# Performance work log

Measured on AMD Instinct MI355X. Metric: run time of the kernel, lower is better.

The kernel has to match this reference:

```python
import jax, jax.numpy as jnp
import numpy as np

TRACT_SPECS = [
    dict(name="x_a", src_size=4096, dst_size=1024, connections=64, seed=42),
    dict(name="x_b", src_size=4096, dst_size=512, connections=64, seed=43),
    dict(name="x_c", src_size=2048, dst_size=512, connections=32, seed=44),
]


def _make_mask(dst_size, src_size, n_conn, seed):
    rng = np.random.RandomState(seed)
    mask = np.zeros((dst_size, src_size), dtype=np.float32)
    for dst in range(dst_size):
        idx = rng.choice(src_size, size=min(n_conn, src_size), replace=False)
        mask[dst, idx] = 1.0
    return jnp.asarray(mask)


def _xavier_uniform(key, dst, src):
    # matches nn.init.xavier_uniform_ for a (dst, src) weight
    limit = float(np.sqrt(6.0 / (dst + src)))
    return jax.random.uniform(key, (dst, src), jnp.float32, -limit, limit)


def setup_inputs() -> dict:
    key = jax.random.key(0)
    keys = jax.random.split(key, 6)
    B, S = 8, 1024
    inp = {}
    for i, spec in enumerate(TRACT_SPECS):
        src, dst = spec["src_size"], spec["dst_size"]
        inp[spec["name"]] = jax.random.normal(keys[i], (B, S, src), jnp.float32)
        inp["w_" + spec["name"][-1]] = _xavier_uniform(keys[3 + i], dst, src)
        inp["m_" + spec["name"][-1]] = _make_mask(dst, src, spec["connections"], spec["seed"])
    return inp


def reference(x_a, x_b, x_c, w_a, w_b, w_c, m_a, m_b, m_c):
    # Each tract: F.linear(x, weight * mask) -> x @ (W*M)^T; then concat on last dim.
    out_a = jnp.einsum("bsi,oi->bso", x_a, w_a * m_a)
    out_b = jnp.einsum("bsi,oi->bso", x_b, w_b * m_b)
    out_c = jnp.einsum("bsi,oi->bso", x_c, w_c * m_c)
    return jnp.concatenate([out_a, out_b, out_c], axis=-1)
```

## Files before the change

kernel.cpp:

```cpp
#include <hip/hip_runtime.h>
#include <hip/hip_fp16.h>
#include <stdint.h>


#define BS_TOTAL 8192
#define SRC_A 4096
#define SRC_B 4096
#define SRC_C 2048
#define DST_A 1024
#define DST_B 512
#define DST_C 512
#define K_A 64
#define K_B 64
#define K_C 32
#define OUT_DIM 2048

#define PAIR_XB_OFF 4096
#define PAIR_XC_OFF 8192
#define PAIR_TOT 10240
#define LDS_BYTES (PAIR_TOT * 8)

typedef float f32x4 __attribute__((ext_vector_type(4)));


__global__ __launch_bounds__(256) void compress_kernel(
    const float* __restrict__ w_a, const float* __restrict__ m_a,
    const float* __restrict__ w_b, const float* __restrict__ m_b,
    const float* __restrict__ w_c, const float* __restrict__ m_c,
    unsigned* __restrict__ pa, unsigned* __restrict__ pb,
    unsigned* __restrict__ pc) {
    __shared__ int s_cnt;
    __shared__ int s_idx[64];
    __shared__ float s_w[64];
    __shared__ int s_bankcnt[16];
    __shared__ int s_bankoff[16];
    __shared__ unsigned s_sorted[64];

    const int blk = blockIdx.x;
    const int t = threadIdx.x;

    const float *w, *m;
    unsigned* p;
    int dst, src_n, K, DST, pair_off;
    if (blk < DST_A) {
        w = w_a; m = m_a; p = pa; dst = blk;
        src_n = SRC_A; K = K_A; DST = DST_A; pair_off = 0;
    } else if (blk < DST_A + DST_B) {
        w = w_b; m = m_b; p = pb; dst = blk - DST_A;
        src_n = SRC_B; K = K_B; DST = DST_B; pair_off = PAIR_XB_OFF;
    } else {
        w = w_c; m = m_c; p = pc; dst = blk - DST_A - DST_B;
        src_n = SRC_C; K = K_C; DST = DST_C; pair_off = PAIR_XC_OFF;
    }

    if (t == 0) s_cnt = 0;
    if (t < 16) s_bankcnt[t] = 0;
    __syncthreads();

    const float* mrow = m + (size_t)dst * src_n;
    const float* wrow = w + (size_t)dst * src_n;
    const int per_thread = src_n >> 8;
    for (int i = 0; i < per_thread; ++i) {
        int e = t + (i << 8);
        float mv = mrow[e];
        if (mv != 0.0f) {
            int pos = atomicAdd(&s_cnt, 1);
            if (pos < 64) {
                s_idx[pos] = e;
                s_w[pos] = wrow[e] * mv;
            }
        }
    }
    __syncthreads();
    int cnt = s_cnt;
    if (cnt > K) cnt = K;

    if (t < cnt) atomicAdd(&s_bankcnt[s_idx[t] & 15], 1);
    __syncthreads();
    if (t == 0) {
        int acc = 0;
        for (int b = 0; b < 16; ++b) {
            s_bankoff[b] = acc;
            acc += s_bankcnt[b];
        }
    }
    __syncthreads();
    if (t < cnt) {
        int idx = s_idx[t];
        int j = atomicAdd(&s_bankoff[idx & 15], 1);
        unsigned hb = (unsigned)__half_as_ushort(__float2half(s_w[t]));
        s_sorted[j] = ((unsigned)(pair_off + idx) << 16) | hb;
    }
    __syncthreads();
    if (t >= cnt && t < K) s_sorted[t] = ((unsigned)pair_off << 16);
    __syncthreads();

    if (t < K) {
        int rot = (K == 64) ? ((dst & 15) << 2) : ((dst & 15) << 1);
        unsigned v = s_sorted[(t + rot) % K];
        p[(((t >> 2) * DST) + dst) * 4 + (t & 3)] = v;
    }
}

__global__ __launch_bounds__(256, 2) void tract_kernel(
    const float* __restrict__ x_a, const float* __restrict__ x_b,
    const float* __restrict__ x_c,
    const unsigned* __restrict__ pa, const unsigned* __restrict__ pb,
    const unsigned* __restrict__ pc,
    float* __restrict__ out) {
    extern __shared__ unsigned xs[];
    const int t = threadIdx.x;
    const size_t r0 = (size_t)blockIdx.x * 4;

    const f32x4* a0 = (const f32x4*)(x_a + (r0 + 0) * SRC_A);
    const f32x4* a1 = (const f32x4*)(x_a + (r0 + 1) * SRC_A);
    const f32x4* a2 = (const f32x4*)(x_a + (r0 + 2) * SRC_A);
    const f32x4* a3 = (const f32x4*)(x_a + (r0 + 3) * SRC_A);
    const f32x4* b0 = (const f32x4*)(x_b + (r0 + 0) * SRC_B);
    const f32x4* b1 = (const f32x4*)(x_b + (r0 + 1) * SRC_B);
    const f32x4* b2 = (const f32x4*)(x_b + (r0 + 2) * SRC_B);
    const f32x4* b3 = (const f32x4*)(x_b + (r0 + 3) * SRC_B);
    const f32x4* c0 = (const f32x4*)(x_c + (r0 + 0) * SRC_C);
    const f32x4* c1 = (const f32x4*)(x_c + (r0 + 1) * SRC_C);
    const f32x4* c2 = (const f32x4*)(x_c + (r0 + 2) * SRC_C);
    const f32x4* c3 = (const f32x4*)(x_c + (r0 + 3) * SRC_C);
    uint4* xs4 = (uint4*)xs;

#pragma unroll
    for (int i = 0; i < 10; ++i) {
        int q = t + (i << 8);
        const f32x4 *s0, *s1, *s2, *s3;
        int qo;
        if (q < 1024)      { s0 = a0; s1 = a1; s2 = a2; s3 = a3; qo = q; }
        else if (q < 2048) { s0 = b0; s1 = b1; s2 = b2; s3 = b3; qo = q - 1024; }
        else               { s0 = c0; s1 = c1; s2 = c2; s3 = c3; qo = q - 2048; }
        f32x4 v0 = s0[qo];
        f32x4 v1 = s1[qo];
        f32x4 v2 = s2[qo];
        f32x4 v3 = s3[qo];
        uint4 w0, w1;
        __half2 h;
        h = __floats2half2_rn(v0.x, v1.x); w0.x = *(unsigned*)&h;
        h = __floats2half2_rn(v2.x, v3.x); w0.y = *(unsigned*)&h;
        h = __floats2half2_rn(v0.y, v1.y); w0.z = *(unsigned*)&h;
        h = __floats2half2_rn(v2.y, v3.y); w0.w = *(unsigned*)&h;
        h = __floats2half2_rn(v0.z, v1.z); w1.x = *(unsigned*)&h;
        h = __floats2half2_rn(v2.z, v3.z); w1.y = *(unsigned*)&h;
        h = __floats2half2_rn(v0.w, v1.w); w1.z = *(unsigned*)&h;
        h = __floats2half2_rn(v2.w, v3.w); w1.w = *(unsigned*)&h;
        xs4[2 * q]     = w0;
        xs4[2 * q + 1] = w1;
    }
    __syncthreads();

    const uint2* xp = (const uint2*)xs;
    float* o0 = out + (r0 + 0) * OUT_DIM;
    float* o1 = out + (r0 + 1) * OUT_DIM;
    float* o2 = out + (r0 + 2) * OUT_DIM;
    float* o3 = out + (r0 + 3) * OUT_DIM;

#define PROC(u) {                                                            \
        uint2 xv = xp[(u) >> 16];                                            \
        float w = __half2float(__ushort_as_half((unsigned short)((u) & 0xffffu))); \
        const __half2 hlo = *(const __half2*)&xv.x;                          \
        const __half2 hhi = *(const __half2*)&xv.y;                          \
        acc0 = fmaf(w, __low2float(hlo), acc0);                              \
        acc1 = fmaf(w, __high2float(hlo), acc1);                             \
        acc2 = fmaf(w, __low2float(hhi), acc2);                              \
        acc3 = fmaf(w, __high2float(hhi), acc3); }

    const uint4* ta = (const uint4*)pa;
    const uint4* tb = (const uint4*)pb;
    const uint4* tc = (const uint4*)pc;

#pragma unroll 1
    for (int o = 0; o < 4; ++o) {
        int dst = t + (o << 8);
        float acc0 = 0.0f, acc1 = 0.0f, acc2 = 0.0f, acc3 = 0.0f;
#pragma unroll
        for (int k4 = 0; k4 < (K_A >> 2); ++k4) {
            uint4 e = ta[k4 * DST_A + dst];
            PROC(e.x) PROC(e.y) PROC(e.z) PROC(e.w)
        }
        __builtin_nontemporal_store(acc0, o0 + dst);
        __builtin_nontemporal_store(acc1, o1 + dst);
        __builtin_nontemporal_store(acc2, o2 + dst);
        __builtin_nontemporal_store(acc3, o3 + dst);
    }
#pragma unroll 1
    for (int o = 0; o < 2; ++o) {
        int dst = t + (o << 8);
        float acc0 = 0.0f, acc1 = 0.0f, acc2 = 0.0f, acc3 = 0.0f;
#pragma unroll
        for (int k4 = 0; k4 < (K_B >> 2); ++k4) {
            uint4 e = tb[k4 * DST_B + dst];
            PROC(e.x) PROC(e.y) PROC(e.z) PROC(e.w)
        }
        __builtin_nontemporal_store(acc0, o0 + DST_A + dst);
        __builtin_nontemporal_store(acc1, o1 + DST_A + dst);
        __builtin_nontemporal_store(acc2, o2 + DST_A + dst);
        __builtin_nontemporal_store(acc3, o3 + DST_A + dst);
    }
#pragma unroll 1
    for (int o = 0; o < 2; ++o) {
        int dst = t + (o << 8);
        float acc0 = 0.0f, acc1 = 0.0f, acc2 = 0.0f, acc3 = 0.0f;
#pragma unroll
        for (int k4 = 0; k4 < (K_C >> 2); ++k4) {
            uint4 e = tc[k4 * DST_C + dst];
            PROC(e.x) PROC(e.y) PROC(e.z) PROC(e.w)
        }
        __builtin_nontemporal_store(acc0, o0 + DST_A + DST_B + dst);
        __builtin_nontemporal_store(acc1, o1 + DST_A + DST_B + dst);
        __builtin_nontemporal_store(acc2, o2 + DST_A + DST_B + dst);
        __builtin_nontemporal_store(acc3, o3 + DST_A + DST_B + dst);
    }
#undef PROC
}

extern "C" void kernel_launch(void* const* d_in, const int* in_sizes, int n_in,
                              void* d_out, int out_size, void* d_ws, size_t ws_size,
                              hipStream_t stream) {
    const float* x_a = (const float*)d_in[0];
    const float* w_a = (const float*)d_in[1];
    const float* m_a = (const float*)d_in[2];
    const float* x_b = (const float*)d_in[3];
    const float* w_b = (const float*)d_in[4];
    const float* m_b = (const float*)d_in[5];
    const float* x_c = (const float*)d_in[6];
    const float* w_c = (const float*)d_in[7];
    const float* m_c = (const float*)d_in[8];
    float* out = (float*)d_out;

    char* ws = (char*)d_ws;
    unsigned* pa = (unsigned*)(ws);
    unsigned* pb = (unsigned*)(ws + 262144);
    unsigned* pc = (unsigned*)(ws + 262144 + 131072);

    static bool configured = false;
    if (!configured) {
        hipFuncSetAttribute(reinterpret_cast<const void*>(&tract_kernel),
                            hipFuncAttributeMaxDynamicSharedMemorySize, LDS_BYTES);
        configured = true;
    }

    compress_kernel<<<DST_A + DST_B + DST_C, 256, 0, stream>>>(
        w_a, m_a, w_b, m_b, w_c, m_c, pa, pb, pc);
    tract_kernel<<<BS_TOTAL / 4, 256, LDS_BYTES, stream>>>(x_a, x_b, x_c, pa, pb, pc, out);
}
```

Before: 411.5 us.

## Split tract kernel into per-tract blocks with smaller LDS footprint

The fused kernel is restructured so each block handles a single tract for 4 rows instead of all three tracts. The LDS tile shrinks from 80KB to 32KB and the grid triples, allowing more resident blocks per CU and better latency hiding. The compress kernel now loads the mask with vector loads and fetches weights only for nonzero entries. In exchange, each block does less work, so launch and sync overhead rise, and the per-block blocks are uneven across tracts.

```diff
diff --git a/kernel.cpp b/kernel.cpp
--- a/kernel.cpp
+++ b/kernel.cpp
@@ -14,11 +14,12 @@
 #define K_B 64
 #define K_C 32
 #define OUT_DIM 2048
-
-#define PAIR_XB_OFF 4096
-#define PAIR_XC_OFF 8192
-#define PAIR_TOT 10240
-#define LDS_BYTES (PAIR_TOT * 8)
+#define ROWS 4
+
+#define NBLK_A (BS_TOTAL / ROWS)
+#define NBLK_B (BS_TOTAL / ROWS)
+#define NBLK_C (BS_TOTAL / ROWS)
+#define LDS_BYTES (SRC_A * 8)
 
 typedef float f32x4 __attribute__((ext_vector_type(4)));
 
@@ -31,7 +32,6 @@
     unsigned* __restrict__ pc) {
     __shared__ int s_cnt;
     __shared__ int s_idx[64];
-    __shared__ float s_w[64];
     __shared__ int s_bankcnt[16];
     __shared__ int s_bankoff[16];
     __shared__ unsigned s_sorted[64];
@@ -41,16 +41,16 @@
 
     const float *w, *m;
     unsigned* p;
-    int dst, src_n, K, DST, pair_off;
+    int dst, src_n, K, DST;
     if (blk < DST_A) {
         w = w_a; m = m_a; p = pa; dst = blk;
-        src_n = SRC_A; K = K_A; DST = DST_A; pair_off = 0;
+        src_n = SRC_A; K = K_A; DST = DST_A;
     } else if (blk < DST_A + DST_B) {
         w = w_b; m = m_b; p = pb; dst = blk - DST_A;
-        src_n = SRC_B; K = K_B; DST = DST_B; pair_off = PAIR_XB_OFF;
+        src_n = SRC_B; K = K_B; DST = DST_B;
     } else {
         w = w_c; m = m_c; p = pc; dst = blk - DST_A - DST_B;
-        src_n = SRC_C; K = K_C; DST = DST_C; pair_off = PAIR_XC_OFF;
+        src_n = SRC_C; K = K_C; DST = DST_C;
     }
 
     if (t == 0) s_cnt = 0;
@@ -59,15 +59,16 @@
 
     const float* mrow = m + (size_t)dst * src_n;
     const float* wrow = w + (size_t)dst * src_n;
-    const int per_thread = src_n >> 8;
-    for (int i = 0; i < per_thread; ++i) {
-        int e = t + (i << 8);
-        float mv = mrow[e];
-        if (mv != 0.0f) {
-            int pos = atomicAdd(&s_cnt, 1);
-            if (pos < 64) {
-                s_idx[pos] = e;
-                s_w[pos] = wrow[e] * mv;
+    const f32x4* m4 = (const f32x4*)mrow;
+    const int nq = src_n >> 10;
+    for (int i = 0; i < nq; ++i) {
+        int q = t + (i << 8);
+        f32x4 mv = m4[q];
+#pragma unroll
+        for (int j = 0; j < 4; ++j) {
+            if (mv[j] != 0.0f) {
+                int pos = atomicAdd(&s_cnt, 1);
+                if (pos < 64) s_idx[pos] = 4 * q + j;
             }
         }
     }
@@ -88,56 +89,50 @@
     if (t < cnt) {
         int idx = s_idx[t];
         int j = atomicAdd(&s_bankoff[idx & 15], 1);
-        unsigned hb = (unsigned)__half_as_ushort(__float2half(s_w[t]));
-        s_sorted[j] = ((unsigned)(pair_off + idx) << 16) | hb;
-    }
-    __syncthreads();
-    if (t >= cnt && t < K) s_sorted[t] = ((unsigned)pair_off << 16);
+        float wv = wrow[idx] * mrow[idx];
+        unsigned hb = (unsigned)__half_as_ushort(__float2half(wv));
+        s_sorted[j] = ((unsigned)idx << 16) | hb;
+    }
+    __syncthreads();
+    if (t >= cnt && t < K) s_sorted[t] = 0u;
     __syncthreads();
 
     if (t < K) {
         int rot = (K == 64) ? ((dst & 15) << 2) : ((dst & 15) << 1);
-        unsigned v = s_sorted[(t + rot) % K];
+        unsigned v = s_sorted[(t + rot) & (K - 1)];
         p[(((t >> 2) * DST) + dst) * 4 + (t & 3)] = v;
     }
 }
 
-__global__ __launch_bounds__(256, 2) void tract_kernel(
-    const float* __restrict__ x_a, const float* __restrict__ x_b,
-    const float* __restrict__ x_c,
-    const unsigned* __restrict__ pa, const unsigned* __restrict__ pb,
-    const unsigned* __restrict__ pc,
-    float* __restrict__ out) {
-    extern __shared__ unsigned xs[];
-    const int t = threadIdx.x;
-    const size_t r0 = (size_t)blockIdx.x * 4;
-
-    const f32x4* a0 = (const f32x4*)(x_a + (r0 + 0) * SRC_A);
-    const f32x4* a1 = (const f32x4*)(x_a + (r0 + 1) * SRC_A);
-    const f32x4* a2 = (const f32x4*)(x_a + (r0 + 2) * SRC_A);
-    const f32x4* a3 = (const f32x4*)(x_a + (r0 + 3) * SRC_A);
-    const f32x4* b0 = (const f32x4*)(x_b + (r0 + 0) * SRC_B);
-    const f32x4* b1 = (const f32x4*)(x_b + (r0 + 1) * SRC_B);
-    const f32x4* b2 = (const f32x4*)(x_b + (r0 + 2) * SRC_B);
-    const f32x4* b3 = (const f32x4*)(x_b + (r0 + 3) * SRC_B);
-    const f32x4* c0 = (const f32x4*)(x_c + (r0 + 0) * SRC_C);
-    const f32x4* c1 = (const f32x4*)(x_c + (r0 + 1) * SRC_C);
-    const f32x4* c2 = (const f32x4*)(x_c + (r0 + 2) * SRC_C);
-    const f32x4* c3 = (const f32x4*)(x_c + (r0 + 3) * SRC_C);
+
+#define PROC(u) {                                                            \
+        uint2 xv = xp[(u) >> 16];                                            \
+        float w = __half2float(__ushort_as_half((unsigned short)((u) & 0xffffu))); \
+        const __half2 hlo = *(const __half2*)&xv.x;                          \
+        const __half2 hhi = *(const __half2*)&xv.y;                          \
+        acc0 = fmaf(w, __low2float(hlo), acc0);                              \
+        acc1 = fmaf(w, __high2float(hlo), acc1);                             \
+        acc2 = fmaf(w, __low2float(hhi), acc2);                              \
+        acc3 = fmaf(w, __high2float(hhi), acc3); }
+
+template <int SRCN, int KQ, int DSTN, int NOUT>
+__device__ __forceinline__ void do_tract(
+    const float* __restrict__ xsrc, const uint4* __restrict__ tab,
+    float* __restrict__ outb,
+    size_t r0, int t, unsigned* xs) {
+    const f32x4* s0 = (const f32x4*)(xsrc + (r0 + 0) * SRCN);
+    const f32x4* s1 = (const f32x4*)(xsrc + (r0 + 1) * SRCN);
+    const f32x4* s2 = (const f32x4*)(xsrc + (r0 + 2) * SRCN);
+    const f32x4* s3 = (const f32x4*)(xsrc + (r0 + 3) * SRCN);
     uint4* xs4 = (uint4*)xs;
 
 #pragma unroll
-    for (int i = 0; i < 10; ++i) {
+    for (int i = 0; i < (SRCN >> 10); ++i) {
         int q = t + (i << 8);
-        const f32x4 *s0, *s1, *s2, *s3;
-        int qo;
-        if (q < 1024)      { s0 = a0; s1 = a1; s2 = a2; s3 = a3; qo = q; }
-        else if (q < 2048) { s0 = b0; s1 = b1; s2 = b2; s3 = b3; qo = q - 1024; }
-        else               { s0 = c0; s1 = c1; s2 = c2; s3 = c3; qo = q - 2048; }
-        f32x4 v0 = s0[qo];
-        f32x4 v1 = s1[qo];
-        f32x4 v2 = s2[qo];
-        f32x4 v3 = s3[qo];
+        f32x4 v0 = s0[q];
+        f32x4 v1 = s1[q];
+        f32x4 v2 = s2[q];
+        f32x4 v3 = s3[q];
         uint4 w0, w1;
         __half2 h;
         h = __floats2half2_rn(v0.x, v1.x); w0.x = *(unsigned*)&h;
@@ -154,32 +149,18 @@
     __syncthreads();
 
     const uint2* xp = (const uint2*)xs;
-    float* o0 = out + (r0 + 0) * OUT_DIM;
-    float* o1 = out + (r0 + 1) * OUT_DIM;
-    float* o2 = out + (r0 + 2) * OUT_DIM;
-    float* o3 = out + (r0 + 3) * OUT_DIM;
-
-#define PROC(u) {                                                            \
-        uint2 xv = xp[(u) >> 16];                                            \
-        float w = __half2float(__ushort_as_half((unsigned short)((u) & 0xffffu))); \
-        const __half2 hlo = *(const __half2*)&xv.x;                          \
-        const __half2 hhi = *(const __half2*)&xv.y;                          \
-        acc0 = fmaf(w, __low2float(hlo), acc0);                              \
-        acc1 = fmaf(w, __high2float(hlo), acc1);                             \
-        acc2 = fmaf(w, __low2float(hhi), acc2);                              \
-        acc3 = fmaf(w, __high2float(hhi), acc3); }
-
-    const uint4* ta = (const uint4*)pa;
-    const uint4* tb = (const uint4*)pb;
-    const uint4* tc = (const uint4*)pc;
+    float* o0 = outb;
+    float* o1 = outb + OUT_DIM;
+    float* o2 = outb + 2 * OUT_DIM;
+    float* o3 = outb + 3 * OUT_DIM;
 
 #pragma unroll 1
-    for (int o = 0; o < 4; ++o) {
+    for (int o = 0; o < NOUT; ++o) {
         int dst = t + (o << 8);
         float acc0 = 0.0f, acc1 = 0.0f, acc2 = 0.0f, acc3 = 0.0f;
 #pragma unroll
-        for (int k4 = 0; k4 < (K_A >> 2); ++k4) {
-            uint4 e = ta[k4 * DST_A + dst];
+        for (int k4 = 0; k4 < KQ; ++k4) {
+            uint4 e = tab[k4 * DSTN + dst];
             PROC(e.x) PROC(e.y) PROC(e.z) PROC(e.w)
         }
         __builtin_nontemporal_store(acc0, o0 + dst);
@@ -187,35 +168,31 @@
         __builtin_nontemporal_store(acc2, o2 + dst);
         __builtin_nontemporal_store(acc3, o3 + dst);
     }
-#pragma unroll 1
-    for (int o = 0; o < 2; ++o) {
-        int dst = t + (o << 8);
-        float acc0 = 0.0f, acc1 = 0.0f, acc2 = 0.0f, acc3 = 0.0f;
-#pragma unroll
-        for (int k4 = 0; k4 < (K_B >> 2); ++k4) {
-            uint4 e = tb[k4 * DST_B + dst];
-            PROC(e.x) PROC(e.y) PROC(e.z) PROC(e.w)
-        }
-        __builtin_nontemporal_store(acc0, o0 + DST_A + dst);
-        __builtin_nontemporal_store(acc1, o1 + DST_A + dst);
-        __builtin_nontemporal_store(acc2, o2 + DST_A + dst);
-        __builtin_nontemporal_store(acc3, o3 + DST_A + dst);
-    }
-#pragma unroll 1
-    for (int o = 0; o < 2; ++o) {
-        int dst = t + (o << 8);
-        float acc0 = 0.0f, acc1 = 0.0f, acc2 = 0.0f, acc3 = 0.0f;
-#pragma unroll
-        for (int k4 = 0; k4 < (K_C >> 2); ++k4) {
-            uint4 e = tc[k4 * DST_C + dst];
-            PROC(e.x) PROC(e.y) PROC(e.z) PROC(e.w)
-        }
-        __builtin_nontemporal_store(acc0, o0 + DST_A + DST_B + dst);
-        __builtin_nontemporal_store(acc1, o1 + DST_A + DST_B + dst);
-        __builtin_nontemporal_store(acc2, o2 + DST_A + DST_B + dst);
-        __builtin_nontemporal_store(acc3, o3 + DST_A + DST_B + dst);
-    }
-#undef PROC
+}
+
+__global__ __launch_bounds__(256) void tract_kernel(
+    const float* __restrict__ x_a, const float* __restrict__ x_b,
+    const float* __restrict__ x_c,
+    const unsigned* __restrict__ pa, const unsigned* __restrict__ pb,
+    const unsigned* __restrict__ pc,
+    float* __restrict__ out) {
+    extern __shared__ unsigned xs[];
+    const int t = threadIdx.x;
+    const int blk = blockIdx.x;
+
+    if (blk < NBLK_A) {
+        size_t r0 = (size_t)blk * ROWS;
+        do_tract<SRC_A, K_A / 4, DST_A, 4>(
+            x_a, (const uint4*)pa, out + r0 * OUT_DIM, r0, t, xs);
+    } else if (blk < NBLK_A + NBLK_B) {
+        size_t r0 = (size_t)(blk - NBLK_A) * ROWS;
+        do_tract<SRC_B, K_B / 4, DST_B, 2>(
+            x_b, (const uint4*)pb, out + r0 * OUT_DIM + DST_A, r0, t, xs);
+    } else {
+        size_t r0 = (size_t)(blk - NBLK_A - NBLK_B) * ROWS;
+        do_tract<SRC_C, K_C / 4, DST_C, 2>(
+            x_c, (const uint4*)pc, out + r0 * OUT_DIM + DST_A + DST_B, r0, t, xs);
+    }
 }
 
 extern "C" void kernel_launch(void* const* d_in, const int* in_sizes, int n_in,
@@ -237,14 +214,8 @@
     unsigned* pb = (unsigned*)(ws + 262144);
     unsigned* pc = (unsigned*)(ws + 262144 + 131072);
 
-    static bool configured = false;
-    if (!configured) {
-        hipFuncSetAttribute(reinterpret_cast<const void*>(&tract_kernel),
-                            hipFuncAttributeMaxDynamicSharedMemorySize, LDS_BYTES);
-        configured = true;
-    }
-
     compress_kernel<<<DST_A + DST_B + DST_C, 256, 0, stream>>>(
         w_a, m_a, w_b, m_b, w_c, m_c, pa, pb, pc);
-    tract_kernel<<<BS_TOTAL / 4, 256, LDS_BYTES, stream>>>(x_a, x_b, x_c, pa, pb, pc, out);
-}
+    tract_kernel<<<NBLK_A + NBLK_B + NBLK_C, 256, LDS_BYTES, stream>>>(
+        x_a, x_b, x_c, pa, pb, pc, out);
+}
```

After: 380.9 us. -7.4%, faster.
